# Kernel optimization log

Hardware: AMD Instinct MI355X
Metric: run time of the kernel (lower is better)

Reference implementation:

```python
import math
import jax, jax.numpy as jnp
import numpy as np

B, S, D, P, H = 8, 512, 1024, 128, 8  # batch, seq_len, dim, phase_dim, num_heads


def _layernorm(v, g, b, eps=1e-5):
    m = jnp.mean(v, axis=-1, keepdims=True)
    var = jnp.mean((v - m) ** 2, axis=-1, keepdims=True)
    return (v - m) * jax.lax.rsqrt(var + eps) * g + b


def setup_inputs() -> dict:
    key = jax.random.key(0)
    ks = jax.random.split(key, 12)
    s = 0.02
    f32 = jnp.float32
    return {
        'x':   jax.random.normal(ks[0], (B, S, D), f32),
        'Wa':  jax.random.normal(ks[1], (D, P), f32) * s,
        'ba':  jnp.zeros((P,), f32),
        'Wp':  jax.random.normal(ks[2], (D, P), f32) * s,
        'bp':  jnp.zeros((P,), f32),
        'g1':  jnp.ones((P,), f32),
        'bt1': jnp.zeros((P,), f32),
        'W1':  jax.random.normal(ks[3], (H, P, 2 * P), f32) * s,
        'bh1': jnp.zeros((H, 2 * P), f32),
        'W2':  jax.random.normal(ks[4], (H, 2 * P, P), f32) * s,
        'bh2': jnp.zeros((H, P), f32),
        'g2':  jnp.ones((P,), f32),
        'bt2': jnp.zeros((P,), f32),
        'Wo':  jax.random.normal(ks[5], (H * P, D), f32) * s,
        'bo':  jnp.zeros((D,), f32),
    }


def reference(x, Wa, ba, Wp, bp, g1, bt1, W1, bh1, W2, bh2, g2, bt2, Wo, bo):
    # amplitude/phase encoding; only the real part is ever used downstream
    amp = jnp.tanh(x @ Wa + ba)                       # [B,S,P]
    ph = jax.nn.sigmoid(x @ Wp + bp) * (2.0 * math.pi)
    real = amp * jnp.cos(ph)                          # [B,S,P]

    xn = _layernorm(real, g1, bt1)                    # shared norm1
    # per-head MLP, vectorized over heads via einsum
    t = jax.nn.gelu(jnp.einsum('bsp,hpq->hbsq', xn, W1) + bh1[:, None, None, :],
                    approximate=False)
    t = jnp.einsum('hbsq,hqp->hbsp', t, W2) + bh2[:, None, None, :]  # [H,B,S,P]

    # per-(head,sample,channel) self cross-correlation of the transformed
    # signal with itself (the conv1d(x, x, groups=batch) trick), padding=S//2,
    # truncated to S lags so it gates elementwise.
    C = H * B * P
    Tc = jnp.transpose(t, (0, 1, 3, 2)).reshape(1, C, S)   # [1, C, S]
    w = Tc.reshape(C, 1, S)                                 # one kernel per channel
    pad = S // 2
    inter = jax.lax.conv_general_dilated(Tc, w, (1,), [(pad, pad)],
                                         feature_group_count=C)  # [1, C, S+1]
    inter = inter[0, :, :S].reshape(H, B, P, S)
    inter = jnp.transpose(inter, (0, 1, 3, 2))              # [H,B,S,P]

    gated = real[None] * jax.nn.sigmoid(inter)              # [H,B,S,P]
    comb = jnp.transpose(gated, (1, 2, 0, 3))               # [B,S,H,P]
    nrm = _layernorm(comb, g2, bt2).reshape(B, S, H * P)    # norm2 per head
    return nrm @ Wo + bo + x
```

## Files before the change

### kernel.cpp

```cpp
#include <hip/hip_runtime.h>
#include <math.h>

typedef __attribute__((ext_vector_type(8))) short bf16x8_t;
typedef __attribute__((ext_vector_type(4))) float f32x4_t;

__device__ __forceinline__ float sigmoidf_(float x){ return 1.f/(1.f+expf(-x)); }
__device__ __forceinline__ float geluf_(float x){ return 0.5f*x*(1.f+erff(x*0.70710678118654752f)); }
__device__ __forceinline__ unsigned short f2bf(float x){
  unsigned int u = __float_as_uint(x);
  return (unsigned short)((u + 0x7fffu + ((u>>16)&1u)) >> 16);
}
__device__ __forceinline__ float bf2f(unsigned short h){
  return __uint_as_float(((unsigned int)h)<<16);
}
__device__ __forceinline__ bf16x8_t ldfrag(const unsigned short* p){
  union { bf16x8_t v; uint2 q[2]; } u;
  u.q[0] = *(const uint2*)p; u.q[1] = *(const uint2*)(p+4); return u.v;
}

__global__ __launch_bounds__(256) void bias_pack(const float* __restrict__ ba,
    const float* __restrict__ bp, float* __restrict__ bcat){
  int t = threadIdx.x; bcat[t] = (t<128)? ba[t] : bp[t-128];
}

__global__ __launch_bounds__(256) void transpose_split(
    const float* __restrict__ src, unsigned short* __restrict__ dhi,
    unsigned short* __restrict__ dlo, int R, int C)
{
  long zoff = (long)blockIdx.z * R * C;
  src += zoff; dhi += zoff; dlo += zoff;
  __shared__ float tile[32][33];
  int c0 = blockIdx.x*32, r0 = blockIdx.y*32;
  int j = threadIdx.x & 31, i0 = threadIdx.x >> 5;
  #pragma unroll
  for (int ii=0; ii<4; ++ii){ int i = i0 + ii*8;
    tile[i][j] = src[(long)(r0+i)*C + c0 + j]; }
  __syncthreads();
  #pragma unroll
  for (int ii=0; ii<4; ++ii){ int i = i0 + ii*8;
    float v = tile[j][i];
    unsigned short h = f2bf(v);
    dhi[(long)(c0+i)*R + r0 + j] = h;
    dlo[(long)(c0+i)*R + r0 + j] = f2bf(v - bf2f(h));
  }
}

template<int EPI>
__global__ __launch_bounds__(256) void gemm_mfma(
    const float* __restrict__ A, const unsigned short* __restrict__ Bhi,
    const unsigned short* __restrict__ Blo,
    const float* __restrict__ bias, const float* __restrict__ resid,
    float* __restrict__ C, int M, int N, int K,
    long sA, long sB, long sBias, long sC)
{
  int z = blockIdx.z;
  A += (long)z*sA; Bhi += (long)z*sB; Blo += (long)z*sB; bias += (long)z*sBias; C += (long)z*sC;
  __shared__ unsigned short As_hi[64][68], As_lo[64][68];
  __shared__ unsigned short Bs_hi[128][68], Bs_lo[128][68];
  const int tid = threadIdx.x;
  const int lane = tid & 63, wv = tid >> 6;
  const int wr = wv >> 1, wc = wv & 1;
  const int mw = wr*32, nw = wc*64;
  const int la = lane & 15, kg = (lane >> 4) << 3;
  const int m0 = blockIdx.x * 64, n0 = blockIdx.y * 128;

  f32x4_t acc[2][4];
  #pragma unroll
  for (int i=0;i<2;++i)
    #pragma unroll
    for (int j=0;j<4;++j) acc[i][j] = (f32x4_t){0.f,0.f,0.f,0.f};

  for (int k0 = 0; k0 < K; k0 += 64) {
    float4 av[4]; uint4 bh4[4], bl4[4];
    #pragma unroll
    for (int r=0;r<4;++r){
      int ia = tid + r*256;
      av[r] = *(const float4*)(A + (long)(m0 + (ia>>4))*K + k0 + ((ia&15)<<2));
      int ib = tid + r*256;
      long bo = (long)(n0 + (ib>>3))*K + k0 + ((ib&7)<<3);
      bh4[r] = *(const uint4*)(Bhi + bo);
      bl4[r] = *(const uint4*)(Blo + bo);
    }
    __syncthreads();
    #pragma unroll
    for (int r=0;r<4;++r){
      int ia = tid + r*256;
      int arow = ia>>4, akc = (ia&15)<<2;
      float4 v = av[r];
      unsigned short h0=f2bf(v.x),h1=f2bf(v.y),h2=f2bf(v.z),h3=f2bf(v.w);
      uint2 whi; whi.x = (unsigned)h0 | ((unsigned)h1<<16); whi.y = (unsigned)h2 | ((unsigned)h3<<16);
      *(uint2*)&As_hi[arow][akc] = whi;
      unsigned short l0=f2bf(v.x-bf2f(h0)),l1=f2bf(v.y-bf2f(h1)),
                     l2=f2bf(v.z-bf2f(h2)),l3=f2bf(v.w-bf2f(h3));
      uint2 wlo; wlo.x = (unsigned)l0 | ((unsigned)l1<<16); wlo.y = (unsigned)l2 | ((unsigned)l3<<16);
      *(uint2*)&As_lo[arow][akc] = wlo;
      int ib = tid + r*256;
      int bn = ib>>3, bkc = (ib&7)<<3;
      uint2 t0; t0.x = bh4[r].x; t0.y = bh4[r].y;
      uint2 t1; t1.x = bh4[r].z; t1.y = bh4[r].w;
      *(uint2*)&Bs_hi[bn][bkc]   = t0;
      *(uint2*)&Bs_hi[bn][bkc+4] = t1;
      uint2 t2; t2.x = bl4[r].x; t2.y = bl4[r].y;
      uint2 t3; t3.x = bl4[r].z; t3.y = bl4[r].w;
      *(uint2*)&Bs_lo[bn][bkc]   = t2;
      *(uint2*)&Bs_lo[bn][bkc+4] = t3;
    }
    __syncthreads();
    #pragma unroll
    for (int kk=0; kk<2; ++kk){
      bf16x8_t ah[2], al[2], bh[4], bl[4];
      #pragma unroll
      for (int mf=0; mf<2; ++mf){
        ah[mf] = ldfrag(&As_hi[mw + mf*16 + la][kk*32 + kg]);
        al[mf] = ldfrag(&As_lo[mw + mf*16 + la][kk*32 + kg]);
      }
      #pragma unroll
      for (int nf=0; nf<4; ++nf){
        bh[nf] = ldfrag(&Bs_hi[nw + nf*16 + la][kk*32 + kg]);
        bl[nf] = ldfrag(&Bs_lo[nw + nf*16 + la][kk*32 + kg]);
      }
      #pragma unroll
      for (int mf=0; mf<2; ++mf)
        #pragma unroll
        for (int nf=0; nf<4; ++nf){
          acc[mf][nf] = __builtin_amdgcn_mfma_f32_16x16x32_bf16(ah[mf], bh[nf], acc[mf][nf], 0,0,0);
          acc[mf][nf] = __builtin_amdgcn_mfma_f32_16x16x32_bf16(ah[mf], bl[nf], acc[mf][nf], 0,0,0);
          acc[mf][nf] = __builtin_amdgcn_mfma_f32_16x16x32_bf16(al[mf], bh[nf], acc[mf][nf], 0,0,0);
        }
    }
  }
  #pragma unroll
  for (int mf=0; mf<2; ++mf){
    int grow0 = m0 + mw + mf*16 + ((lane>>4)<<2);
    #pragma unroll
    for (int nf=0; nf<4; ++nf){
      int gcol = n0 + nw + nf*16 + la;
      float bsv = bias[gcol];
      if (EPI==4){
        float4 o;
        o.x = acc[mf][nf][0] + bsv; o.y = acc[mf][nf][1] + bsv;
        o.z = acc[mf][nf][2] + bsv; o.w = acc[mf][nf][3] + bsv;
        *(float4*)(C + (long)gcol*M + grow0) = o;
      } else {
        #pragma unroll
        for (int r=0;r<4;++r){
          int grow = grow0 + r;
          float v = acc[mf][nf][r] + bsv;
          if (EPI==1) v = geluf_(v);
          if (EPI==2) v += resid[(long)grow*N + gcol];
          C[(long)grow*N + gcol] = v;
        }
      }
    }
  }
}

__global__ __launch_bounds__(256) void encode_ln_kernel(
    const float* __restrict__ E, const float* __restrict__ g1, const float* __restrict__ bt1,
    float* __restrict__ realp, float* __restrict__ xnp)
{
  int wv = threadIdx.x >> 6, lane = threadIdx.x & 63;
  long row = (long)blockIdx.x*4 + wv;
  const float* e = E + row*256;
  int p = lane*2;
  float2 a = *(const float2*)(e + p);
  float2 f = *(const float2*)(e + 128 + p);
  const float TWO_PI = 6.28318530717958647692f;
  float r0 = tanhf(a.x) * cosf(TWO_PI * sigmoidf_(f.x));
  float r1 = tanhf(a.y) * cosf(TWO_PI * sigmoidf_(f.y));
  float s = r0+r1, ss = r0*r0 + r1*r1;
  #pragma unroll
  for (int m=1;m<64;m<<=1){ s += __shfl_xor(s,m,64); ss += __shfl_xor(ss,m,64); }
  float mean = s * (1.f/128.f);
  float var  = ss * (1.f/128.f) - mean*mean;
  float inv  = rsqrtf(var + 1e-5f);
  float x0 = (r0-mean)*inv*g1[p]   + bt1[p];
  float x1 = (r1-mean)*inv*g1[p+1] + bt1[p+1];
  *(float2*)(realp + row*128 + p) = make_float2(r0,r1);
  *(float2*)(xnp   + row*128 + p) = make_float2(x0,x1);
}

__global__ __launch_bounds__(256) void autocorr_kernel(
    const float* __restrict__ tT, float* __restrict__ sig)
{
  __shared__ float vp[4][968];
  int bidx = blockIdx.x;
  int p4 = bidx & 31; int hb = bidx >> 5; int b = hb & 7, h = hb >> 3;
  float* vflat = &vp[0][0];
  for (int i = threadIdx.x; i < 4*968; i += 256) vflat[i] = 0.f;
  __syncthreads();
  const float* tp = tT + ((long)(h*128 + p4*4))*4096 + b*512;
  for (int idx = threadIdx.x; idx < 2048; idx += 256) {
    int c = idx >> 9, s = idx & 511;
    vp[c][s + ((s>>3)<<1)] = tp[(long)c*4096 + s];
  }
  __syncthreads();
  int wv = threadIdx.x >> 6, lane = threadIdx.x & 63;
  const float* V = vp[wv];
  int lb = lane*4;
  float acc[4] = {0,0,0,0};
  float cur[8], nxt[8], aa[8];
  #pragma unroll
  for (int u=0;u<8;u+=2){ int li = lb+u; *(float2*)&cur[u] = *(const float2*)&V[li + ((li>>3)<<1)]; }
  for (int t0=0; t0<512; t0+=8){
    #pragma unroll
    for (int u=0;u<8;u+=2){ int li = t0+8+lb+u; *(float2*)&nxt[u] = *(const float2*)&V[li + ((li>>3)<<1)]; }
    #pragma unroll
    for (int u=0;u<8;u+=2){ int li = t0+u; *(float2*)&aa[u] = *(const float2*)&V[li + ((li>>3)<<1)]; }
    #pragma unroll
    for (int u=0;u<8;++u){
      float a = aa[u];
      #pragma unroll
      for (int j=0;j<4;++j){
        int w = u+j;
        float wl = (w<8)? cur[w] : nxt[w-8];
        acc[j] = fmaf(a, wl, acc[j]);
      }
    }
    #pragma unroll
    for (int u=0;u<8;++u) cur[u]=nxt[u];
  }
  float r256 = 0.f;
  #pragma unroll
  for (int u=0;u<4;++u){
    int t = lb + u; int t2 = t + 256;
    r256 = fmaf(V[t + ((t>>3)<<1)], V[t2 + ((t2>>3)<<1)], r256);
  }
  #pragma unroll
  for (int m=1;m<64;m<<=1) r256 += __shfl_xor(r256, m, 64);
  float* sp = sig + ((long)(h*4096 + b*512))*128 + p4*4 + wv;
  #pragma unroll
  for (int j=0;j<4;++j){
    int lam = lb + j;
    float bv = sigmoidf_(acc[j]);
    sp[(long)(256+lam)*128] = bv;
    if (lam > 0) sp[(long)(256-lam)*128] = bv;
  }
  if (lane == 0) sp[0] = sigmoidf_(r256);
}

__global__ __launch_bounds__(256) void gate_ln_kernel(
    const float* __restrict__ realp, const float* __restrict__ sig,
    const float* __restrict__ g2, const float* __restrict__ bt2,
    float* __restrict__ y)
{
  int wv = threadIdx.x >> 6, lane = threadIdx.x & 63;
  long r = (long)blockIdx.x*4 + wv;
  int h = (int)(r >> 12);
  long rem = r & 4095;
  int p = lane*2;
  float2 rv = *(const float2*)(realp + rem*128 + p);
  float2 sv = *(const float2*)(sig + r*128 + p);
  float a0 = rv.x*sv.x, a1 = rv.y*sv.y;
  float s = a0+a1, ss = a0*a0+a1*a1;
  #pragma unroll
  for (int m=1;m<64;m<<=1){ s += __shfl_xor(s,m,64); ss += __shfl_xor(ss,m,64); }
  float mean = s*(1.f/128.f);
  float var  = ss*(1.f/128.f) - mean*mean;
  float inv  = rsqrtf(var+1e-5f);
  float y0 = (a0-mean)*inv*g2[p]   + bt2[p];
  float y1 = (a1-mean)*inv*g2[p+1] + bt2[p+1];
  *(float2*)(y + rem*1024 + h*128 + p) = make_float2(y0,y1);
}

extern "C" void kernel_launch(void* const* d_in, const int* in_sizes, int n_in,
                              void* d_out, int out_size, void* d_ws, size_t ws_size,
                              hipStream_t stream)
{
  const float* x   = (const float*)d_in[0];
  const float* Wa  = (const float*)d_in[1];
  const float* ba  = (const float*)d_in[2];
  const float* Wp  = (const float*)d_in[3];
  const float* bp  = (const float*)d_in[4];
  const float* g1  = (const float*)d_in[5];
  const float* bt1 = (const float*)d_in[6];
  const float* W1  = (const float*)d_in[7];
  const float* bh1 = (const float*)d_in[8];
  const float* W2  = (const float*)d_in[9];
  const float* bh2 = (const float*)d_in[10];
  const float* g2  = (const float*)d_in[11];
  const float* bt2 = (const float*)d_in[12];
  const float* Wo  = (const float*)d_in[13];
  const float* bo  = (const float*)d_in[14];

  char* p = (char*)d_ws;
  auto alloc = [&](size_t bytes)->char*{ char* r = p; p += (bytes + 255) & ~(size_t)255; return r; };
  float* bcat = (float*)alloc(256*4);
  unsigned short* WcatT_hi = (unsigned short*)alloc(256*1024*2);
  unsigned short* WcatT_lo = (unsigned short*)alloc(256*1024*2);
  unsigned short* W1T_hi   = (unsigned short*)alloc(8*256*128*2);
  unsigned short* W1T_lo   = (unsigned short*)alloc(8*256*128*2);
  unsigned short* W2T_hi   = (unsigned short*)alloc(8*128*256*2);
  unsigned short* W2T_lo   = (unsigned short*)alloc(8*128*256*2);
  unsigned short* WoT_hi   = (unsigned short*)alloc(1024*1024*2);
  unsigned short* WoT_lo   = (unsigned short*)alloc(1024*1024*2);
  float* E     = (float*)alloc((size_t)4096*256*4);
  float* realp = (float*)alloc((size_t)4096*128*4);
  float* xnp   = (float*)alloc((size_t)4096*128*4);
  float* hid   = (float*)alloc((size_t)8*4096*256*4);
  float* tbuf  = (float*)alloc((size_t)8*128*4096*4);
  float* sigb  = hid;
  float* ybuf  = tbuf;
  float* out   = (float*)d_out;

  bias_pack<<<1,256,0,stream>>>(ba,bp,bcat);
  transpose_split<<<dim3(4,32,1),256,0,stream>>>(Wa, WcatT_hi, WcatT_lo, 1024,128);
  transpose_split<<<dim3(4,32,1),256,0,stream>>>(Wp, WcatT_hi+131072, WcatT_lo+131072, 1024,128);
  transpose_split<<<dim3(8,4,8),256,0,stream>>>(W1, W1T_hi, W1T_lo, 128,256);
  transpose_split<<<dim3(4,8,8),256,0,stream>>>(W2, W2T_hi, W2T_lo, 256,128);
  transpose_split<<<dim3(32,32,1),256,0,stream>>>(Wo, WoT_hi, WoT_lo, 1024,1024);

  gemm_mfma<0><<<dim3(64,2,1),256,0,stream>>>(x, WcatT_hi, WcatT_lo, bcat, nullptr, E,
                                              4096,256,1024, 0,0,0,0);
  encode_ln_kernel<<<1024,256,0,stream>>>(E,g1,bt1,realp,xnp);
  gemm_mfma<1><<<dim3(64,2,8),256,0,stream>>>(xnp, W1T_hi, W1T_lo, bh1, nullptr, hid,
                                              4096,256,128, 0, (long)256*128, 256, (long)4096*256);
  gemm_mfma<4><<<dim3(64,1,8),256,0,stream>>>(hid, W2T_hi, W2T_lo, bh2, nullptr, tbuf,
                                              4096,128,256, (long)4096*256, (long)128*256, 128, (long)128*4096);
  autocorr_kernel<<<2048,256,0,stream>>>(tbuf, sigb);
  gate_ln_kernel<<<8192,256,0,stream>>>(realp, sigb, g2, bt2, ybuf);
  gemm_mfma<2><<<dim3(64,8,1),256,0,stream>>>(ybuf, WoT_hi, WoT_lo, bo, x, out,
                                              4096,1024,1024, 0,0,0,0);
}
```

Before: 263.2 us.

## Compute autocorrelation lags with bf16 split-precision MFMA instead of scalar FMAs

The autocorrelation kernel now converts each channel to bf16 hi/lo pairs in shared memory, stored as four shifted copies. It builds Toeplitz-style fragments so a 16x16x32 MFMA computes 256 lags in 17 k-blocks, using three MFMAs per block (hi*hi, hi*lo, lo*hi) to approximate fp32 accuracy. This replaces the per-lane scalar FMA sliding-window loop with matrix-core work. The cost is more shared memory, extra conversion and store work, and slightly reduced precision from dropping the lo*lo term.

```diff
diff --git a/kernel.cpp b/kernel.cpp
--- a/kernel.cpp
+++ b/kernel.cpp
@@ -16,6 +16,9 @@
 __device__ __forceinline__ bf16x8_t ldfrag(const unsigned short* p){
   union { bf16x8_t v; uint2 q[2]; } u;
   u.q[0] = *(const uint2*)p; u.q[1] = *(const uint2*)(p+4); return u.v;
+}
+__device__ __forceinline__ bf16x8_t ldfrag16(const unsigned short* p){
+  union { bf16x8_t v; uint4 q; } u; u.q = *(const uint4*)p; return u.v;
 }
 
 __global__ __launch_bounds__(256) void bias_pack(const float* __restrict__ ba,
@@ -180,59 +183,80 @@
   *(float2*)(xnp   + row*128 + p) = make_float2(x0,x1);
 }
 
+__device__ __forceinline__ int hi_off_(int d){ return d ? (512 + d*1280) : 0; }
+__device__ __forceinline__ int lo_off_(int d){ return d ? (1152 + d*1280) : 896; }
+__device__ __forceinline__ int physpad_(int m){ return m + ((m >> 6) << 3); }
+
 __global__ __launch_bounds__(256) void autocorr_kernel(
     const float* __restrict__ tT, float* __restrict__ sig)
 {
-  __shared__ float vp[4][968];
+  __shared__ __align__(16) unsigned short pool[4][5632];
+  const int tid = threadIdx.x;
+  const int wv = tid >> 6, lane = tid & 63;
   int bidx = blockIdx.x;
   int p4 = bidx & 31; int hb = bidx >> 5; int b = hb & 7, h = hb >> 3;
-  float* vflat = &vp[0][0];
-  for (int i = threadIdx.x; i < 4*968; i += 256) vflat[i] = 0.f;
+
+  unsigned int* pz = (unsigned int*)&pool[0][0];
+  for (int i = tid; i < 4*5632/2; i += 256) pz[i] = 0u;
   __syncthreads();
-  const float* tp = tT + ((long)(h*128 + p4*4))*4096 + b*512;
-  for (int idx = threadIdx.x; idx < 2048; idx += 256) {
-    int c = idx >> 9, s = idx & 511;
-    vp[c][s + ((s>>3)<<1)] = tp[(long)c*4096 + s];
+
+  unsigned short* P = pool[wv];
+  {
+    const float* tp = tT + ((long)(h*128 + p4*4 + wv))*4096 + b*512;
+    for (int i = lane; i < 512; i += 64) {
+      float v = tp[i];
+      unsigned short hh = f2bf(v);
+      unsigned short ll = f2bf(v - bf2f(hh));
+      #pragma unroll
+      for (int d = 0; d < 4; ++d) {
+        int ph = physpad_(i + 16 - d);
+        P[hi_off_(d) + ph] = hh;
+        P[lo_off_(d) + ph] = ll;
+      }
+    }
   }
   __syncthreads();
-  int wv = threadIdx.x >> 6, lane = threadIdx.x & 63;
-  const float* V = vp[wv];
-  int lb = lane*4;
-  float acc[4] = {0,0,0,0};
-  float cur[8], nxt[8], aa[8];
-  #pragma unroll
-  for (int u=0;u<8;u+=2){ int li = lb+u; *(float2*)&cur[u] = *(const float2*)&V[li + ((li>>3)<<1)]; }
-  for (int t0=0; t0<512; t0+=8){
-    #pragma unroll
-    for (int u=0;u<8;u+=2){ int li = t0+8+lb+u; *(float2*)&nxt[u] = *(const float2*)&V[li + ((li>>3)<<1)]; }
-    #pragma unroll
-    for (int u=0;u<8;u+=2){ int li = t0+u; *(float2*)&aa[u] = *(const float2*)&V[li + ((li>>3)<<1)]; }
-    #pragma unroll
-    for (int u=0;u<8;++u){
-      float a = aa[u];
-      #pragma unroll
-      for (int j=0;j<4;++j){
-        int w = u+j;
-        float wl = (w<8)? cur[w] : nxt[w-8];
-        acc[j] = fmaf(a, wl, acc[j]);
-      }
-    }
-    #pragma unroll
-    for (int u=0;u<8;++u) cur[u]=nxt[u];
-  }
+
+  const int la = lane & 15, kg8 = (lane >> 4) << 3;
+  f32x4_t acc = (f32x4_t){0.f,0.f,0.f,0.f};
+  for (int kb = 0; kb < 17; ++kb) {
+    int qA = kb*32 + kg8 + la*16 + 16;
+    int phA = physpad_(qA);
+    bf16x8_t Ah = ldfrag16(P + phA);
+    bf16x8_t Al = ldfrag16(P + 896 + phA);
+    int qB = kb*32 + kg8 + 16 - la;
+    int d = qB & 3;
+    int r0 = qB - d, r1 = r0 + 4;
+    int ph0 = physpad_(r0), ph1 = physpad_(r1);
+    int hio = hi_off_(d), loo = lo_off_(d);
+    union { bf16x8_t v; uint2 q[2]; } ub, vb;
+    ub.q[0] = *(const uint2*)(P + hio + ph0);
+    ub.q[1] = *(const uint2*)(P + hio + ph1);
+    vb.q[0] = *(const uint2*)(P + loo + ph0);
+    vb.q[1] = *(const uint2*)(P + loo + ph1);
+    acc = __builtin_amdgcn_mfma_f32_16x16x32_bf16(Ah, ub.v, acc, 0,0,0);
+    acc = __builtin_amdgcn_mfma_f32_16x16x32_bf16(Ah, vb.v, acc, 0,0,0);
+    acc = __builtin_amdgcn_mfma_f32_16x16x32_bf16(Al, ub.v, acc, 0,0,0);
+  }
+
   float r256 = 0.f;
   #pragma unroll
-  for (int u=0;u<4;++u){
-    int t = lb + u; int t2 = t + 256;
-    r256 = fmaf(V[t + ((t>>3)<<1)], V[t2 + ((t2>>3)<<1)], r256);
-  }
-  #pragma unroll
-  for (int m=1;m<64;m<<=1) r256 += __shfl_xor(r256, m, 64);
+  for (int u = 0; u < 4; ++u) {
+    int t = lane*4 + u;
+    int p1 = physpad_(t + 16), p2 = physpad_(t + 272);
+    float v1 = bf2f(P[p1]) + bf2f(P[896 + p1]);
+    float v2 = bf2f(P[p2]) + bf2f(P[896 + p2]);
+    r256 = fmaf(v1, v2, r256);
+  }
+  #pragma unroll
+  for (int m = 1; m < 64; m <<= 1) r256 += __shfl_xor(r256, m, 64);
+
   float* sp = sig + ((long)(h*4096 + b*512))*128 + p4*4 + wv;
-  #pragma unroll
-  for (int j=0;j<4;++j){
-    int lam = lb + j;
-    float bv = sigmoidf_(acc[j]);
+  int arow = (lane >> 4) << 2;
+  #pragma unroll
+  for (int rr = 0; rr < 4; ++rr) {
+    int lam = (arow + rr)*16 + la;
+    float bv = sigmoidf_(acc[rr]);
     sp[(long)(256+lam)*128] = bv;
     if (lam > 0) sp[(long)(256-lam)*128] = bv;
   }
```

Result: faster. 257.6 us (-2.1%).
